# Performance work log

Measured on AMD Instinct MI355X. Metric: run time of the kernel, lower is better.

Reference implementation:

```python
import jax, jax.numpy as jnp
import numpy as np
import math

B, L, NH, HD = 2, 2048, 8, 128
C = NH * HD            # hidden size
K = 3                  # short_conv_L
EMB, ORDER = 33, 64    # hyena filter emb_dim / order


def setup_inputs() -> dict:
    key = jax.random.key(0)
    ks = jax.random.split(key, 10)
    f32 = jnp.float32
    return {
        "query_layer": jax.random.normal(ks[0], (L, B, NH, HD), f32),
        "key_layer": jax.random.normal(ks[1], (L, B, NH, HD), f32),
        "value_layer": jax.random.normal(ks[2], (L, B, NH, HD), f32),
        # depthwise short conv params: [3(qkv), C, 1, K] / [3, C]
        "short_conv_weight": jax.random.normal(ks[3], (3, C, 1, K), f32) * 0.3,
        "short_conv_bias": jax.random.normal(ks[4], (3, C), f32) * 0.02,
        # D term of the long conv, shape [head_dim]
        "long_conv_bias": jax.random.normal(ks[5], (HD,), f32) * 0.1,
        # hyena filter MLP (torch Linear convention: W [out, in])
        "lin0_w": jax.random.normal(ks[6], (ORDER, EMB), f32) * (1.0 / np.sqrt(EMB)),
        "lin0_b": jnp.zeros((ORDER,), f32),
        "lin1_w": jax.random.normal(ks[7], (ORDER, ORDER), f32) * (1.0 / np.sqrt(ORDER)),
        "lin1_b": jnp.zeros((ORDER,), f32),
        "lin2_w": jax.random.normal(ks[8], (ORDER, ORDER), f32) * (1.0 / np.sqrt(ORDER)),
        "lin2_b": jnp.zeros((ORDER,), f32),
        "freq": jnp.ones((1, ORDER), f32),  # Sin activation freq (w=1), shared across layers
        "final_w": jax.random.normal(ks[9], (HD, ORDER), f32) * (1.0 / np.sqrt(ORDER)),
        # exponential modulation decay rates, [1,1,HD], as initialized in the module
        "mod_weight": jnp.linspace(math.log(0.01) / 1.5, math.log(0.01) / 0.3, HD,
                                   dtype=f32)[None, None],
    }


def _depthwise_conv(x, w, b):
    # x [B,C,L], w [C,1,K], b [C]; causal: pad K-1 both sides, keep first L
    y = jax.lax.conv_general_dilated(
        x, w, window_strides=(1,), padding=[(K - 1, K - 1)],
        feature_group_count=C, dimension_numbers=("NCH", "OIH", "NCH"))
    return y[..., :L] + b[None, :, None]


def _hyena_filter(lin0_w, lin0_b, lin1_w, lin1_b, lin2_w, lin2_b, freq, final_w, mod_weight):
    t = jnp.linspace(0.0, 1.0, L)[None, :, None]              # [1,L,1]
    bands = (EMB - 1) // 2
    w_ang = 2.0 * jnp.pi * jnp.linspace(0.0, L - 1.0, L) / L  # [L]
    f = jnp.linspace(1e-4, bands - 1.0, bands)                # [bands]
    theta = w_ang[:, None] * f[None, :]                       # [L,bands]; z = exp(-1j f w)
    z = jnp.concatenate([t[0], jnp.cos(theta), -jnp.sin(theta)], axis=-1)[None]  # [1,L,EMB]
    h = jnp.sin(freq * (z @ lin0_w.T + lin0_b))
    h = jnp.sin(freq * (h @ lin1_w.T + lin1_b))
    h = jnp.sin(freq * (h @ lin2_w.T + lin2_b))
    h = h @ final_w.T                                         # [1,L,HD]
    h = h * jnp.exp(-t * jnp.abs(mod_weight))                 # exponential modulation
    return h[0].T                                             # [HD, L]


def _fftconv_heads(k, kern, D, q, v):
    # mirrors fftconv_heads_ref with head_dim=NH: channels split as (h=HD, d=NH)
    b = k.shape[0]
    kr = k.reshape(b, HD, NH, L).transpose(0, 2, 1, 3)  # b nh hd L  (d1 axis)
    vr = v.reshape(b, HD, NH, L).transpose(0, 2, 1, 3)  # b nh hd L  (d2 axis)
    qr = q.reshape(b, HD, NH, L).transpose(0, 2, 1, 3)  # b nh hd L
    kv = kr[:, :, None] * vr[:, None]                   # [b, nh, nh, hd, L]
    n = 2 * L
    kv_f = jnp.fft.rfft(kv, n=n) / n
    kern_f = jnp.fft.rfft(kern, n=n)                    # [HD, n//2+1]
    y = jnp.fft.irfft(kv_f * kern_f, n=n, norm="forward")[..., :L]
    out = y + kv * D[:, None]                           # D over head_dim axis
    out = (out * qr[:, :, None]).sum(axis=1)            # _mul_sum over d1 -> [b, nh, hd, L]
    return out.transpose(0, 2, 1, 3).reshape(b, C, L)   # 'b d2 h l -> b (h d2) l'


def reference(query_layer, key_layer, value_layer, short_conv_weight, short_conv_bias,
              long_conv_bias, lin0_w, lin0_b, lin1_w, lin1_b, lin2_w, lin2_b,
              freq, final_w, mod_weight):
    # 'sq b np hn -> b (np hn) sq'
    q = jnp.transpose(query_layer, (1, 2, 3, 0)).reshape(B, C, L)
    k = jnp.transpose(key_layer, (1, 2, 3, 0)).reshape(B, C, L)
    v = jnp.transpose(value_layer, (1, 2, 3, 0)).reshape(B, C, L)
    q = _depthwise_conv(q, short_conv_weight[0], short_conv_bias[0])
    k = _depthwise_conv(k, short_conv_weight[1], short_conv_bias[1])
    v = _depthwise_conv(v, short_conv_weight[2], short_conv_bias[2])
    filt = _hyena_filter(lin0_w, lin0_b, lin1_w, lin1_b, lin2_w, lin2_b,
                         freq, final_w, mod_weight)
    # module calls fftconv_heads_ref(k=value, ..., q=query, v=key)
    y = _fftconv_heads(v, filt, long_conv_bias, q=q, v=k)
    # 'b (np hn) sq -> b np sq hn'
    return y.reshape(B, NH, HD, L).transpose(0, 1, 3, 2)
```

## Files before the change

### kernel.cpp

```cpp
#include <hip/hip_runtime.h>
#include <stdint.h>

#define L_SEQ 2048
#define B_SZ 2
#define NHH 8
#define HDD 128
#define C_SZ 1024
#define EMB_D 33
#define ORD 64
#define BANDS 16
#define FSTRIDE (L_SEQ + 256)
#define FRS_S 2600
#define FRS_FILL 2176

typedef _Float16 f16;
typedef f16 f16x8 __attribute__((ext_vector_type(8)));
typedef float f32x4 __attribute__((ext_vector_type(4)));

__global__ void filter_kernel(const float* __restrict__ w0, const float* __restrict__ b0,
                              const float* __restrict__ w1, const float* __restrict__ b1,
                              const float* __restrict__ w2, const float* __restrict__ b2,
                              const float* __restrict__ fr, const float* __restrict__ wf,
                              const float* __restrict__ md, const float* __restrict__ Dv,
                              float* __restrict__ filt) {
  int tid = threadIdx.x;
  int o = tid & 63;
  int lq = tid >> 6;
  int l = blockIdx.x * 4 + lq;

  if (blockIdx.x < 128) filt[(size_t)blockIdx.x * FSTRIDE + tid] = 0.0f;

  __shared__ float zs[4][EMB_D];
  __shared__ float hs[4][ORD];
  __shared__ float gs[4][ORD];

  float t = (float)l / (float)(L_SEQ - 1);
  float wang = 6.2831853071795864f * (float)l / (float)L_SEQ;
  const float fstep = (15.0f - 1e-4f) / 15.0f;

  if (o == 0) zs[lq][0] = t;
  if (o >= 1 && o < 1 + BANDS) {
    int j = o - 1;
    float fj = 1e-4f + fstep * (float)j;
    zs[lq][1 + j] = cosf(wang * fj);
  }
  if (o >= 1 + BANDS && o < 1 + 2 * BANDS) {
    int j = o - 1 - BANDS;
    float fj = 1e-4f + fstep * (float)j;
    zs[lq][1 + BANDS + j] = -sinf(wang * fj);
  }
  __syncthreads();

  float fo = fr[o];
  float a = b0[o];
  for (int e = 0; e < EMB_D; ++e) a += zs[lq][e] * w0[o * EMB_D + e];
  hs[lq][o] = sinf(fo * a);
  __syncthreads();

  a = b1[o];
  for (int e = 0; e < ORD; ++e) a += hs[lq][e] * w1[o * ORD + e];
  gs[lq][o] = sinf(fo * a);
  __syncthreads();

  a = b2[o];
  for (int e = 0; e < ORD; ++e) a += gs[lq][e] * w2[o * ORD + e];
  float h3 = sinf(fo * a);
  __syncthreads();
  hs[lq][o] = h3;
  __syncthreads();

  #pragma unroll
  for (int pass = 0; pass < 2; ++pass) {
    int hd = pass * 64 + o;
    float acc = 0.0f;
    for (int e = 0; e < ORD; ++e) acc += hs[lq][e] * wf[hd * ORD + e];
    float val = acc * expf(-t * fabsf(md[hd]));
    if (l == 0) val += Dv[hd];
    filt[(size_t)hd * FSTRIDE + 256 + l] = val;
  }
}

#define TLC 64
__global__ void shortconv_kernel(const float* __restrict__ q_in,
                                 const float* __restrict__ k_in,
                                 const float* __restrict__ v_in,
                                 const float* __restrict__ scw,
                                 const float* __restrict__ scb,
                                 float* __restrict__ AqT, f16* __restrict__ Akt16,
                                 f16* __restrict__ Avt16) {
  int bid = blockIdx.x;
  int lt = bid & 31;
  int np = (bid >> 5) & 7;
  int b = bid >> 8;
  int l0 = lt * TLC;
  int tid = threadIdx.x;

  __shared__ float xs[TLC + 2][HDD + 4];
  __shared__ float wcs[HDD][4];

  const float* ins[3] = {q_in, k_in, v_in};

  for (int tsr = 0; tsr < 3; ++tsr) {
    const float* x = ins[tsr];
    if (tid < HDD) {
      int c = np * HDD + tid;
      wcs[tid][0] = scw[(tsr * C_SZ + c) * 3 + 0];
      wcs[tid][1] = scw[(tsr * C_SZ + c) * 3 + 1];
      wcs[tid][2] = scw[(tsr * C_SZ + c) * 3 + 2];
      wcs[tid][3] = scb[tsr * C_SZ + c];
    }
    for (int idx = tid; idx < (TLC + 2) * HDD; idx += 256) {
      int row = idx >> 7, hn = idx & 127;
      int l = l0 - 2 + row;
      float val = 0.0f;
      if (l >= 0) val = x[(((size_t)l * B_SZ + b) * NHH + np) * HDD + hn];
      xs[row][hn] = val;
    }
    __syncthreads();

    int n1 = tid & 7;
    int lp = tid >> 3;
    for (int hdi = 0; hdi < 16; ++hdi) {
      int hn = hdi * 8 + n1;
      float cw0 = wcs[hn][0], cw1 = wcs[hn][1], cw2 = wcs[hn][2], cb = wcs[hn][3];
      int hd = np * 16 + hdi;
      #pragma unroll
      for (int half = 0; half < 2; ++half) {
        int ll = half * 32 + lp;
        float y = cb + cw0 * xs[ll][hn] + cw1 * xs[ll + 1][hn]
                     + cw2 * xs[ll + 2][hn];
        int l = l0 + ll;
        if (tsr == 0) {
          AqT[(((size_t)b * HDD + hd) * NHH + n1) * L_SEQ + l] = y;
        } else {
          int ch = l >> 7, m = l & 127;
          int off = (n1 << 8) | ((m << 1) ^ (n1 << 4));
          char* base = (tsr == 1) ? (char*)Akt16 : (char*)Avt16;
          *(f16*)(base + ((((size_t)(b * HDD + hd)) * 16 + ch) << 11) + off) = (f16)y;
        }
      }
    }
    __syncthreads();
  }
}

__global__ void __launch_bounds__(256, 3)
hyena_main(const float* __restrict__ AqT, const f16* __restrict__ Akt16,
           const f16* __restrict__ Avt16, const float* __restrict__ filt,
           float* __restrict__ out) {
  int bid = blockIdx.x;
  int pr = bid & 7;
  int hd = (bid >> 3) & 127;
  int b  = bid >> 10;
  int tid = threadIdx.x;
  int w = tid >> 6;
  int lane = tid & 63;
  int r = lane & 15;
  int p = lane >> 4;
  int a = (15 - r) & 7;

  __shared__ f16 FRS[8][FRS_S];
  __shared__ f16 AV[2][1024];
  __shared__ f16 AK[2][1024];

  const float* frow = filt + (size_t)hd * FSTRIDE + 256;
  const char* avtg = (const char*)Avt16 + (((size_t)(b * HDD + hd)) * 16 << 11);
  const char* aktg = (const char*)Akt16 + (((size_t)(b * HDD + hd)) * 16 << 11);
  const float* aqtb = AqT + ((size_t)b * HDD + hd) * NHH * L_SEQ;
  int np = hd >> 4, hnb = (hd & 15) * 8;

  for (int aa = 0; aa < 8; ++aa)
    for (int z = tid; z < FRS_FILL; z += 256)
      FRS[aa][z] = (f16)frow[2047 - z - aa];

  f32x4 acc[2][4];

  auto dma = [&](int c, int bi) {
    const char* srcb = (w >> 1) ? aktg : avtg;
    f16* dstb = (w >> 1) ? &AK[bi][(w & 1) * 512] : &AV[bi][(w & 1) * 512];
    const char* src = srcb + ((size_t)c << 11) + (w & 1) * 1024 + lane * 16;
    __builtin_amdgcn_global_load_lds((const unsigned int*)src,
                                     (unsigned int*)dstb, 16, 0, 0);
  };

  auto unit = [&](int lt, int c, int bi) {
    int dy = 2047 - (lt - c) * 128;
    int zb = dy - r - a + p * 8 - 112 + 16 * (3 - w);
    f16x8 f[6];
    #pragma unroll
    for (int j = 0; j < 6; ++j)
      f[j] = *(const f16x8*)&FRS[a][zb + 32 * j];
    int ky = r & 7;
    __builtin_amdgcn_s_setprio(1);
    #pragma unroll
    for (int s = 0; s < 4; ++s) {
      f16x8 kf = *(const f16x8*)&AK[bi][ky * 128 + ((s * 32 + p * 8) ^ (ky * 8))];
      #pragma unroll
      for (int nt = 0; nt < 4; ++nt) {
        int vy = nt * 2 + (r >> 3);
        f16x8 vf = *(const f16x8*)&AV[bi][vy * 128 + ((s * 32 + p * 8) ^ (vy * 8))];
        f16x8 bf = vf * kf;
        acc[0][nt] = __builtin_amdgcn_mfma_f32_16x16x32_f16(
            f[s + 2], bf, acc[0][nt], 0, 0, 0);
        acc[1][nt] = __builtin_amdgcn_mfma_f32_16x16x32_f16(
            f[s], bf, acc[1][nt], 0, 0, 0);
      }
    }
    __builtin_amdgcn_s_setprio(0);
  };

  auto epilogue = [&](int lt) {
    int l0 = lt * 128;
    int hi = r >> 3;
    int n2 = r & 7;
    #pragma unroll
    for (int mi = 0; mi < 2; ++mi) {
      int mt = w + 4 * mi;
      float4 qv[4];
      #pragma unroll
      for (int nt = 0; nt < 4; ++nt)
        qv[nt] = *(const float4*)(aqtb + (size_t)(nt * 2 + hi) * L_SEQ
                                  + l0 + mt * 16 + p * 4);
      #pragma unroll
      for (int reg = 0; reg < 4; ++reg) {
        float pv = qv[0][reg] * acc[mi][0][reg] + qv[1][reg] * acc[mi][1][reg]
                 + qv[2][reg] * acc[mi][2][reg] + qv[3][reg] * acc[mi][3][reg];
        pv += __shfl_xor(pv, 8, 64);
        if (r < 8) {
          int i = mt * 16 + p * 4 + reg;
          out[(((size_t)b * NHH + np) * L_SEQ + (l0 + i)) * HDD + hnb + n2] = pv;
        }
      }
    }
  };

  auto run_pass = [&](int lt, int NC) {
    #pragma unroll
    for (int mi = 0; mi < 2; ++mi)
      #pragma unroll
      for (int nt = 0; nt < 4; ++nt)
        acc[mi][nt] = f32x4{0.f, 0.f, 0.f, 0.f};
    dma(0, 0);
    for (int c = 0; c < NC; ++c) {
      __syncthreads();
      if (c + 1 < NC) dma(c + 1, (c + 1) & 1);
      unit(lt, c, c & 1);
    }
    epilogue(lt);
    __syncthreads();
  };

  run_pass(pr, pr + 1);
  run_pass(15 - pr, 16 - pr);
}

extern "C" void kernel_launch(void* const* d_in, const int* in_sizes, int n_in,
                              void* d_out, int out_size, void* d_ws, size_t ws_size,
                              hipStream_t stream) {
  const float* q_in = (const float*)d_in[0];
  const float* k_in = (const float*)d_in[1];
  const float* v_in = (const float*)d_in[2];
  const float* scw  = (const float*)d_in[3];
  const float* scb  = (const float*)d_in[4];
  const float* Dv   = (const float*)d_in[5];
  const float* w0   = (const float*)d_in[6];
  const float* b0   = (const float*)d_in[7];
  const float* w1   = (const float*)d_in[8];
  const float* b1   = (const float*)d_in[9];
  const float* w2   = (const float*)d_in[10];
  const float* b2   = (const float*)d_in[11];
  const float* fr   = (const float*)d_in[12];
  const float* wf   = (const float*)d_in[13];
  const float* md   = (const float*)d_in[14];

  float* ws   = (float*)d_ws;
  float* filt = ws;
  float* AqT  = ws + (size_t)HDD * FSTRIDE;
  f16*   Akt16 = (f16*)(AqT + (size_t)B_SZ * HDD * L_SEQ * NHH);
  f16*   Avt16 = Akt16 + (size_t)B_SZ * HDD * 16 * 1024;

  filter_kernel<<<512, 256, 0, stream>>>(w0, b0, w1, b1, w2, b2, fr, wf, md, Dv, filt);
  shortconv_kernel<<<512, 256, 0, stream>>>(q_in, k_in, v_in, scw, scb, AqT, Akt16, Avt16);
  hyena_main<<<2048, 256, 0, stream>>>(AqT, Akt16, Avt16, filt, (float*)d_out);
}
```

Measured before the change: 163.2 us.

## Triple-buffer async LDS loads, vectorize filter staging, and remap block indices

Turns the double-buffered global_load_lds pipeline into a three-stage ring. Explicit vmcnt waits let one chunk stay in flight while the current chunk is processed, so a full __syncthreads no longer exposes load latency each iteration. The filter-to-FRS fill now uses float4 loads with reversed f16x4 stores instead of scalar conversions, and FRS padding shrinks to make room for the extra buffer. The block index mapping is reordered so consecutive blocks cover different head dims and batches rather than the pr passes of one channel, which changes L2 locality and load balance. The extra shared memory may cut occupancy, and the hand-written waitcnt logic is fragile; the bi2 variable is dead code.

```diff
diff --git a/kernel.cpp b/kernel.cpp
--- a/kernel.cpp
+++ b/kernel.cpp
@@ -1,5 +1,6 @@
 #include <hip/hip_runtime.h>
 #include <stdint.h>
+#include <string.h>
 
 #define L_SEQ 2048
 #define B_SZ 2
@@ -10,11 +11,12 @@
 #define ORD 64
 #define BANDS 16
 #define FSTRIDE (L_SEQ + 256)
-#define FRS_S 2600
+#define FRS_S 2568
 #define FRS_FILL 2176
 
 typedef _Float16 f16;
 typedef f16 f16x8 __attribute__((ext_vector_type(8)));
+typedef f16 f16x4 __attribute__((ext_vector_type(4)));
 typedef float f32x4 __attribute__((ext_vector_type(4)));
 
 __global__ void filter_kernel(const float* __restrict__ w0, const float* __restrict__ b0,
@@ -149,9 +151,9 @@
            const f16* __restrict__ Avt16, const float* __restrict__ filt,
            float* __restrict__ out) {
   int bid = blockIdx.x;
-  int pr = bid & 7;
-  int hd = (bid >> 3) & 127;
-  int b  = bid >> 10;
+  int pr = bid >> 8;
+  int hd = bid & 127;
+  int b  = (bid >> 7) & 1;
   int tid = threadIdx.x;
   int w = tid >> 6;
   int lane = tid & 63;
@@ -160,8 +162,8 @@
   int a = (15 - r) & 7;
 
   __shared__ f16 FRS[8][FRS_S];
-  __shared__ f16 AV[2][1024];
-  __shared__ f16 AK[2][1024];
+  __shared__ f16 AV[3][1024];
+  __shared__ f16 AK[3][1024];
 
   const float* frow = filt + (size_t)hd * FSTRIDE + 256;
   const char* avtg = (const char*)Avt16 + (((size_t)(b * HDD + hd)) * 16 << 11);
@@ -169,9 +171,15 @@
   const float* aqtb = AqT + ((size_t)b * HDD + hd) * NHH * L_SEQ;
   int np = hd >> 4, hnb = (hd & 15) * 8;
 
-  for (int aa = 0; aa < 8; ++aa)
-    for (int z = tid; z < FRS_FILL; z += 256)
-      FRS[aa][z] = (f16)frow[2047 - z - aa];
+  for (int aa = 0; aa < 8; ++aa) {
+    for (int z4 = tid * 4; z4 < FRS_FILL; z4 += 1024) {
+      const float* s = frow + (2044 - aa - z4);
+      float4 v;
+      __builtin_memcpy(&v, s, 16);
+      f16x4 o = {(f16)v.w, (f16)v.z, (f16)v.y, (f16)v.x};
+      *(f16x4*)&FRS[aa][z4] = o;
+    }
+  }
 
   f32x4 acc[2][4];
 
@@ -241,10 +249,19 @@
       for (int nt = 0; nt < 4; ++nt)
         acc[mi][nt] = f32x4{0.f, 0.f, 0.f, 0.f};
     dma(0, 0);
+    if (NC > 1) dma(1, 1);
     for (int c = 0; c < NC; ++c) {
-      __syncthreads();
-      if (c + 1 < NC) dma(c + 1, (c + 1) & 1);
-      unit(lt, c, c & 1);
+      if (c + 1 < NC)
+        asm volatile("s_waitcnt vmcnt(1) lgkmcnt(0)" ::: "memory");
+      else
+        asm volatile("s_waitcnt vmcnt(0) lgkmcnt(0)" ::: "memory");
+      __builtin_amdgcn_s_barrier();
+      __builtin_amdgcn_sched_barrier(0);
+      if (c + 2 < NC) {
+        int bi2 = c + 2; bi2 -= (bi2 >= 3) ? 3 : 0; bi2 -= (bi2 >= 3) ? 3 : 0;
+        dma(c + 2, (c + 2) % 3);
+      }
+      unit(lt, c, c % 3);
     }
     epilogue(lt);
     __syncthreads();
```

Measured after the change: 148.4 us. -9.1%, faster.
